# Optimization experiments

Hardware: AMD Instinct MI355X
Metric: run time of the kernel (lower is better)

## Reference

```python
import jax, jax.numpy as jnp
import numpy as np

B, C, N, V, W, D = 4, 64, 8, 32, 32, 256  # spa_dim = D


def _ln(x, g, b, eps=1e-5):
    m = jnp.mean(x, -1, keepdims=True)
    v = jnp.mean((x - m) ** 2, -1, keepdims=True)
    return (x - m) * jax.lax.rsqrt(v + eps) * g + b


def _tokens(x):
    # (b, c, n, v, w) -> (b*n, v*w, c)
    b, c, n, v, w = x.shape
    return x.transpose(0, 2, 3, 4, 1).reshape(b * n, v * w, c)


def setup_inputs() -> dict:
    key = jax.random.key(0)
    ks = jax.random.split(key, 8)
    fea_lf = jax.random.normal(ks[0], (B, C, N, V, W), jnp.float32)
    fea_hf = jax.random.normal(ks[1], (B, C, N, V, W), jnp.float32)
    W_in = jax.random.normal(ks[2], (C, D), jnp.float32) / np.sqrt(C)
    W_kv = jax.random.normal(ks[3], (C, 2 * D), jnp.float32) / np.sqrt(C)
    gamma = jnp.ones((D,), jnp.float32)
    beta = jnp.zeros((D,), jnp.float32)
    g2 = jnp.ones((D,), jnp.float32)
    b2 = jnp.zeros((D,), jnp.float32)
    W1 = jax.random.normal(ks[4], (D, 2 * D), jnp.float32) / np.sqrt(D)
    W2 = jax.random.normal(ks[5], (2 * D, D), jnp.float32) / np.sqrt(2 * D)
    W_out = jax.random.normal(ks[6], (D, C), jnp.float32) / np.sqrt(D)
    return {"fea_lf": fea_lf, "fea_hf": fea_hf, "W_in": W_in, "W_kv": W_kv,
            "gamma": gamma, "beta": beta, "g2": g2, "b2": b2,
            "W1": W1, "W2": W2, "W_out": W_out}


def reference(fea_lf, fea_hf, W_in, W_kv, gamma, beta, g2, b2, W1, W2, W_out):
    b, c, n, v, w = fea_lf.shape
    S = v * w
    tok_q = _tokens(fea_lf)   # (bn, S, c)
    tok_kv = _tokens(fea_hf)  # (bn, S, c)
    q = _ln(tok_q @ W_in, gamma, beta)              # (bn, S, D)
    kv = tok_kv @ W_kv
    k, vtok = jnp.split(kv, 2, axis=-1)
    k = _ln(k, gamma, beta)                          # shared LayerNorm (self.norm)
    # NOTE: original has no 1/sqrt(d) scaling on scores.
    score = jnp.einsum('bqd,bkd->bqk', q, k)         # (bn, S, S)
    mask = jnp.tril(jnp.ones((S, S), bool))
    score = jnp.where(mask, score, jnp.float32(-1e15))
    p = jax.nn.softmax(score, axis=-1)
    att = jnp.einsum('bqk,bkd->bqd', p, vtok)        # (bn, S, D)
    h = jax.nn.relu(_ln(att, g2, b2) @ W1) @ W2      # FFN (dropout=0)
    epi = h + vtok
    out = epi @ W_out                                # (bn, S, c)
    return out.reshape(b, n, v, w, c).transpose(0, 4, 1, 2, 3)
```

## Files before the change

### kernel.cpp

```cpp
#include <hip/hip_runtime.h>

typedef short bf16x8 __attribute__((ext_vector_type(8)));
typedef _Float16 f16x8 __attribute__((ext_vector_type(8)));
typedef float f32x4 __attribute__((ext_vector_type(4)));
typedef unsigned short u16;
typedef unsigned short u16x4 __attribute__((ext_vector_type(4)));

#define MFMA(a, b, c) __builtin_amdgcn_mfma_f32_16x16x32_bf16(a, b, c, 0, 0, 0)
#define MFMAH(a, b, c) __builtin_amdgcn_mfma_f32_16x16x32_f16(a, b, c, 0, 0, 0)

__device__ __forceinline__ u16 f2b(float f) {
    union { float f; unsigned u; } x{f};
    unsigned r = (x.u + 0x7FFFu + ((x.u >> 16) & 1u)) >> 16;
    return (u16)r;
}
__device__ __forceinline__ float b2f(u16 h) {
    union { unsigned u; float f; } x{((unsigned)h) << 16};
    return x.f;
}
__device__ __forceinline__ u16 f2h(float f) {
    _Float16 h = (_Float16)f;
    return *reinterpret_cast<u16*>(&h);
}
__device__ __forceinline__ float h2f(u16 h) {
    _Float16 v = *reinterpret_cast<_Float16*>(&h);
    return (float)v;
}
__device__ __forceinline__ float red16_sum(float v) {
#pragma unroll
    for (int m = 1; m < 16; m <<= 1) v += __shfl_xor(v, m, 64);
    return v;
}
__device__ __forceinline__ float red16_max(float v) {
#pragma unroll
    for (int m = 1; m < 16; m <<= 1) v = fmaxf(v, __shfl_xor(v, m, 64));
    return v;
}
__device__ __forceinline__ void gl_lds16(const void* g, void* l) {
    __builtin_amdgcn_global_load_lds(
        (const __attribute__((address_space(1))) unsigned int*)(g),
        (__attribute__((address_space(3))) unsigned int*)(l), 16, 0, 0);
}


__global__ __launch_bounds__(256) void wconv_kernel(
    const float* __restrict__ W1, const float* __restrict__ W2,
    const float* __restrict__ Wo, const float* __restrict__ Win,
    const float* __restrict__ Wkv, u16* __restrict__ w1T,
    u16* __restrict__ w2T, u16* __restrict__ woT, u16* __restrict__ wfrag) {
    int id = blockIdx.x * 256 + threadIdx.x;
    if (id < 131072) {
        int n = id >> 8, k = id & 255;
        w1T[id] = f2b(W1[k * 512 + n]);
    } else if (id < 262144) {
        int j = id - 131072;
        int n = j >> 9, k = j & 511;
        w2T[j] = f2b(W2[k * 256 + n]);
    } else if (id < 278528) {
        int j = id - 262144;
        int n = j >> 8, k = j & 255;
        woT[j] = f2b(Wo[k * 64 + n]);
    } else if (id < 290816) {
        int fid = id - 278528;
        int arr = fid >> 11;
        int e = fid & 2047;
        int ntck = e >> 6, ln = e & 63;
        int lr = ln & 15, lg2 = ln >> 4;
        int nt = ntck >> 1, ck = ntck & 1;
        int d = nt * 16 + lr;
#pragma unroll
        for (int j = 0; j < 8; j++) {
            int c = ck * 32 + lg2 * 8 + j;
            float x;
            if (arr < 2)       x = Win[c * 256 + d];
            else if (arr < 4)  x = Wkv[c * 512 + d];
            else               x = Wkv[c * 512 + 256 + d];
            u16 h = f2b(x);
            u16 v = (arr & 1) ? f2b(x - b2f(h)) : h;
            wfrag[arr * 16384 + e * 8 + j] = v;
        }
    }
}

#define PJ_AH 0
#define PJ_AL 16384
#define PJ_WREG 32768
#define PJ_WORK 98304
__global__ __launch_bounds__(512, 1) void proj_kernel(
    const float* __restrict__ lf, const float* __restrict__ hf,
    const u16* __restrict__ wqg, const u16* __restrict__ wkg,
    const u16* __restrict__ wvg, const float* __restrict__ gamma,
    const float* __restrict__ beta, u16* __restrict__ qf_,
    u16* __restrict__ kf_, u16* __restrict__ vT) {
    extern __shared__ char sm[];
    const int tid = threadIdx.x;
    const int wave = tid >> 6, lane = tid & 63, lr = lane & 15, lg = lane >> 4;
    const int st = blockIdx.x, bn = blockIdx.y;
    const int b = bn >> 3, n = bn & 7;
    const int s0 = st * 128;
    const size_t baseF = (size_t)b * 524288 + (size_t)n * 1024 + s0;

    float gam[16], bet[16];
#pragma unroll
    for (int nt = 0; nt < 16; nt++) {
        gam[nt] = gamma[nt * 16 + lr];
        bet[nt] = beta[nt * 16 + lr];
    }

    auto stage32 = [&](const float* srcbase, int chalf) {
#pragma unroll
        for (int call = 0; call < 2; call++) {
            int unit = call * 8 + wave;
            int obase = unit << 10;
            int e = unit * 256 + lane * 4;
            int cl = e >> 7, si = e & 127;
            gl_lds16(srcbase + (size_t)(chalf * 32 + cl) * 8192 + si,
                     sm + PJ_WORK + obase);
        }
    };
    auto stageW = [&](const u16* wsrc) {
#pragma unroll
        for (int call = 0; call < 8; call++) {
            int obase = (call * 8 + wave) << 10;
            gl_lds16((const char*)wsrc + obase + lane * 16, sm + PJ_WREG + obase);
        }
    };
    auto buildA = [&](int slotbase) {
        int g = wave >> 1;
        int s = ((wave & 1) << 6) | lane;
        float x[8];
#pragma unroll
        for (int cc = 0; cc < 8; cc++)
            x[cc] = *(const float*)(sm + PJ_WORK + ((g * 8 + cc) << 9) + (s << 2));
        bf16x8 ph, pl;
#pragma unroll
        for (int cc = 0; cc < 8; cc++) {
            u16 h = f2b(x[cc]);
            ph[cc] = (short)h;
            pl[cc] = (short)f2b(x[cc] - b2f(h));
        }
        int slp = (slotbase + g) ^ (s & 7);
        *(bf16x8*)(sm + PJ_AH + (s << 7) + (slp << 4)) = ph;
        *(bf16x8*)(sm + PJ_AL + (s << 7) + (slp << 4)) = pl;
    };
    auto loadA = [&](bf16x8* aH, bf16x8* aL) {
        int tl = wave * 16 + lr;
#pragma unroll
        for (int ck = 0; ck < 2; ck++) {
            int off = (tl << 7) + ((((ck << 2) | lg) ^ (tl & 7)) << 4);
            aH[ck] = *(const bf16x8*)(sm + PJ_AH + off);
            aL[ck] = *(const bf16x8*)(sm + PJ_AL + off);
        }
    };
    auto pass3 = [&](const bf16x8* aH, const bf16x8* aL, f32x4* acc) {
#pragma unroll
        for (int nt = 0; nt < 16; nt++) acc[nt] = (f32x4){0.f, 0.f, 0.f, 0.f};
#pragma unroll
        for (int nt = 0; nt < 16; nt++) {
#pragma unroll
            for (int ck = 0; ck < 2; ck++) {
                int wo = (((nt << 1) | ck) << 10) + (lane << 4);
                bf16x8 bh = *(const bf16x8*)(sm + PJ_WREG + wo);
                bf16x8 bl = *(const bf16x8*)(sm + PJ_WREG + 32768 + wo);
                acc[nt] = MFMA(aH[ck], bh, acc[nt]);
                acc[nt] = MFMA(aL[ck], bh, acc[nt]);
                acc[nt] = MFMA(aH[ck], bl, acc[nt]);
            }
        }
    };
    auto lnstats = [&](const f32x4* acc, float* mean, float* rs) {
#pragma unroll
        for (int r = 0; r < 4; r++) {
            float s1 = 0.f, s2 = 0.f;
#pragma unroll
            for (int nt = 0; nt < 16; nt++) {
                float xv = acc[nt][r];
                s1 += xv; s2 += xv * xv;
            }
            s1 = red16_sum(s1);
            s2 = red16_sum(s2);
            float mn = s1 * (1.f / 256.f);
            float var = s2 * (1.f / 256.f) - mn * mn;
            mean[r] = mn;
            rs[r] = rsqrtf(var + 1e-5f);
        }
    };
    auto emit = [&](const f32x4* acc, const float* mean, const float* rs,
                    u16* dst) {
        char* bw = sm + PJ_WORK + wave * 4096;
        const int gtok = bn * 1024 + s0 + wave * 16;
#pragma unroll
        for (int hh = 0; hh < 2; hh++) {
#pragma unroll
            for (int ntl = 0; ntl < 8; ntl++) {
                int nt = hh * 8 + ntl;
#pragma unroll
                for (int r = 0; r < 4; r++) {
                    float y = (acc[nt][r] - mean[r]) * rs[r] * gam[nt] + bet[nt];
                    int tl = lg * 4 + r;
                    int dl = ntl * 16 + lr;
                    int sl = dl >> 3;
                    *(u16*)(bw + tl * 256 + ((sl ^ ((tl >> 2) & 3)) << 4) +
                            (dl & 7) * 2) = f2h(y);
                }
            }
#pragma unroll
            for (int p = 0; p < 4; p++) {
                int row = lane >> 2, slq = (lane & 3) + p * 4;
                bf16x8 v8 = *(const bf16x8*)(bw + row * 256 +
                                             ((slq ^ ((row >> 2) & 3)) << 4));
                *(bf16x8*)(dst + (size_t)(gtok + row) * 256 + hh * 128 +
                           slq * 8) = v8;
            }
        }
    };

    f32x4 acc[16];
    float mean[4], rs[4];
    bf16x8 aH[2], aL[2];

    stage32(lf + baseF, 0);  __syncthreads();
    buildA(0);               __syncthreads();
    stage32(lf + baseF, 1);
    stageW(wqg);             __syncthreads();
    buildA(4);               __syncthreads();
    loadA(aH, aL);
    pass3(aH, aL, acc);
    lnstats(acc, mean, rs);  __syncthreads();
    stageW(wkg);
    emit(acc, mean, rs, qf_);
    __syncthreads();
    stage32(hf + baseF, 0);  __syncthreads();
    buildA(0);               __syncthreads();
    stage32(hf + baseF, 1);  __syncthreads();
    buildA(4);               __syncthreads();
    loadA(aH, aL);
    pass3(aH, aL, acc);
    lnstats(acc, mean, rs);  __syncthreads();
    stageW(wvg);
    emit(acc, mean, rs, kf_);
    __syncthreads();
    pass3(aH, aL, acc);
#pragma unroll
    for (int nt = 0; nt < 16; nt++) {
        u16x4 pv;
#pragma unroll
        for (int r = 0; r < 4; r++) pv[r] = f2h(acc[nt][r]);
        *(u16x4*)(vT + ((size_t)(bn * 256) + nt * 16 + lr) * 1024 + s0 +
                  wave * 16 + lg * 4) = pv;
    }
}

__global__ __launch_bounds__(256) void attn_kernel(
    const u16* __restrict__ qf_, const u16* __restrict__ kf_,
    const u16* __restrict__ vT, const float* __restrict__ g2,
    const float* __restrict__ b2, u16* __restrict__ lnatt) {
    extern __shared__ char smem[];
    const int tid = threadIdx.x;
    const int wave = tid >> 6, lane = tid & 63, lr = lane & 15, lg = lane >> 4;
    const int idx = blockIdx.x;
    const int j = idx & 255;
    const int bn = j & 31, si = j >> 5;
    const int strip = (idx >= 256) ? (15 - si) : si;
    const int qr0 = strip * 64 + wave * 16;
    const int nk = 2 * strip + 2;
    u16* Pw = (u16*)(smem + 65536 + wave * 1280);

    f16x8 qf[8];
    {
        const size_t off = ((size_t)(bn * 1024 + qr0 + lr)) * 256 + lg * 8;
#pragma unroll
        for (int ck = 0; ck < 8; ck++)
            qf[ck] = *(const f16x8*)(qf_ + off + ck * 32);
    }
    f16x8 onesb;
    {
        _Float16 v1 = (lr == 0) ? (_Float16)1.0f : (_Float16)0.0f;
#pragma unroll
        for (int q = 0; q < 8; q++) onesb[q] = v1;
    }

    const int srl = lane >> 5, ss = lane & 31;
    const int vdl = lane >> 2, vg = lane & 3;
    auto stage = [&](int buf, int kt) {
        const int kv0 = kt << 5;
        char* baseK = smem + buf * 16384;
        char* baseV = smem + 32768 + buf * 16384;
#pragma unroll
        for (int ii = 0; ii < 4; ii++) {
            int u = wave * 4 + ii;
            int r = u * 2 + srl;
            size_t go = (((size_t)((bn << 10) + kv0 + r)) << 8) +
                        (unsigned)((ss ^ (r & 7)) << 3);
            gl_lds16(kf_ + go, baseK + u * 1024);
            int d = u * 16 + vdl;
            size_t gv = (((size_t)((bn << 8) + d)) << 10) + kv0 +
                        (unsigned)((vg ^ ((d >> 1) & 3)) << 3);
            gl_lds16(vT + gv, baseV + u * 1024);
        }
    };

    f32x4 o[16];
#pragma unroll
    for (int i = 0; i < 16; i++) o[i] = (f32x4){0.f, 0.f, 0.f, 0.f};
    f32x4 ol = (f32x4){0.f, 0.f, 0.f, 0.f};
    float m[4] = {-INFINITY, -INFINITY, -INFINITY, -INFINITY};

    stage(0, 0);
    __syncthreads();
    for (int kt = 0; kt < nk; kt++) {
        const int cur = kt & 1;
        if (kt + 1 < nk) stage(cur ^ 1, kt + 1);
        if ((kt << 5) <= qr0 + 15) {
            const char* kb = smem + cur * 16384;
            f32x4 sc0 = (f32x4){0.f, 0.f, 0.f, 0.f};
            f32x4 sc1 = (f32x4){0.f, 0.f, 0.f, 0.f};
#pragma unroll
            for (int ck = 0; ck < 8; ck++) {
                int sw = ((ck * 4 + lg) ^ (lr & 7)) << 4;
                int a0 = lr * 512 + sw;
                f16x8 k0 = *(const f16x8*)(kb + a0);
                f16x8 k1 = *(const f16x8*)(kb + a0 + 8192);
                sc0 = MFMAH(qf[ck], k0, sc0);
                sc1 = MFMAH(qf[ck], k1, sc1);
            }
            float scl[4];
            const int kvb = kt << 5;
#pragma unroll
            for (int r = 0; r < 4; r++) {
                int qi = qr0 + lg * 4 + r;
                float s0v = (kvb + lr > qi) ? -1e30f : sc0[r];
                float s1v = (kvb + 16 + lr > qi) ? -1e30f : sc1[r];
                float tm = red16_max(fmaxf(s0v, s1v));
                float mn = fmaxf(m[r], tm);
                scl[r] = __expf(m[r] - mn);
                m[r] = mn;
                int row = lg * 4 + r;
                Pw[row * 40 + lr] = f2h(__expf(s0v - mn));
                Pw[row * 40 + 16 + lr] = f2h(__expf(s1v - mn));
            }
#pragma unroll
            for (int f = 0; f < 16; f++) {
                f32x4 t = o[f];
                t[0] *= scl[0]; t[1] *= scl[1]; t[2] *= scl[2]; t[3] *= scl[3];
                o[f] = t;
            }
            ol[0] *= scl[0]; ol[1] *= scl[1]; ol[2] *= scl[2]; ol[3] *= scl[3];
            f16x8 pa = *(const f16x8*)((const char*)Pw + lr * 80 + lg * 16);
            const char* vb = smem + 32768 + cur * 16384;
#pragma unroll
            for (int db = 0; db < 16; db++) {
                int d = db * 16 + lr;
                f16x8 vf = *(const f16x8*)(vb + d * 64 +
                                           ((lg ^ ((lr >> 1) & 3)) << 4));
                o[db] = MFMAH(pa, vf, o[db]);
            }
            ol = MFMAH(pa, onesb, ol);
        }
        __syncthreads();
    }
    float linv[4];
#pragma unroll
    for (int r = 0; r < 4; r++) linv[r] = 1.f / __shfl(ol[r], lane & 48, 64);
#pragma unroll
    for (int f = 0; f < 16; f++) {
        o[f][0] *= linv[0]; o[f][1] *= linv[1];
        o[f][2] *= linv[2]; o[f][3] *= linv[3];
    }
    float gv[16], bv[16];
#pragma unroll
    for (int f = 0; f < 16; f++) {
        gv[f] = g2[f * 16 + lr];
        bv[f] = b2[f * 16 + lr];
    }
#pragma unroll
    for (int r = 0; r < 4; r++) {
        float s1 = 0.f, s2 = 0.f;
#pragma unroll
        for (int f = 0; f < 16; f++) { float x = o[f][r]; s1 += x; s2 += x * x; }
        s1 = red16_sum(s1);
        s2 = red16_sum(s2);
        float mean = s1 * (1.f / 256.f);
        float var = s2 * (1.f / 256.f) - mean * mean;
        float rsv = rsqrtf(var + 1e-5f);
        size_t row = (size_t)(bn * 1024 + qr0 + lg * 4 + r) * 256;
#pragma unroll
        for (int f = 0; f < 16; f++)
            lnatt[row + f * 16 + lr] = f2b((o[f][r] - mean) * rsv * gv[f] + bv[f]);
    }
}

template <int K, int NB, int MODE>
__global__ __launch_bounds__(512) void gemmB_kernel(
    const u16* __restrict__ A, const u16* __restrict__ BT,
    u16* __restrict__ outb, const u16* __restrict__ vTr,
    float* __restrict__ outf, int ldOut) {
    extern __shared__ char bsm[];
    const int tid = threadIdx.x;
    const int wave = tid >> 6, lane = tid & 63, lr = lane & 15, lg = lane >> 4;
    constexpr int K2 = K * 2;
    constexpr int BN = NB * 16;
    constexpr int TILE = BN * K2;
    const int m0 = blockIdx.x * 128 + wave * 16;
    const int n0 = blockIdx.y * BN;
    {
        const char* bsrc = (const char*)(BT + (size_t)n0 * K);
        constexpr int ITER = TILE / (512 * 16);
#pragma unroll
        for (int it = 0; it < ITER; it++) {
            int o = (it * 512 + tid) * 16;
            int col = o / K2;
            int slot = (o % K2) >> 4;
            int src = col * K2 + ((slot ^ (col & 7)) << 4);
            gl_lds16(bsrc + src, bsm + o);
        }
    }
    __syncthreads();
    f32x4 acc[NB];
#pragma unroll
    for (int nb = 0; nb < NB; nb++) acc[nb] = (f32x4){0.f, 0.f, 0.f, 0.f};
    const u16* ap = A + (size_t)(m0 + lr) * K + lg * 8;
#pragma unroll
    for (int kc = 0; kc < K; kc += 32) {
        bf16x8 a = *(const bf16x8*)(ap + kc);
        int ks = (kc >> 3) + lg;
#pragma unroll
        for (int nb = 0; nb < NB; nb++) {
            int c = nb * 16 + lr;
            bf16x8 bv = *(const bf16x8*)(bsm + c * K2 + ((ks ^ (c & 7)) << 4));
            acc[nb] = MFMA(a, bv, acc[nb]);
        }
    }
    const int g = m0 + lg * 4;
    if (MODE == 0) {
#pragma unroll
        for (int nb = 0; nb < NB; nb++)
#pragma unroll
            for (int r = 0; r < 4; r++)
                outb[(size_t)(g + r) * ldOut + n0 + nb * 16 + lr] =
                    f2b(fmaxf(acc[nb][r], 0.f));
    } else if (MODE == 1) {
        int bn = g >> 10, s = g & 1023;
#pragma unroll
        for (int nb = 0; nb < NB; nb++) {
            int dd = n0 + nb * 16 + lr;
            u16x4 vv = *(const u16x4*)(vTr + ((size_t)bn * 256 + dd) * 1024 + s);
#pragma unroll
            for (int r = 0; r < 4; r++)
                outb[(size_t)(g + r) * 256 + dd] = f2b(acc[nb][r] + h2f(vv[r]));
        }
    } else {
        int bn = g >> 10, s = g & 1023;
        int bb = bn >> 3, nn = bn & 7;
#pragma unroll
        for (int nb = 0; nb < NB; nb++) {
            int cc = n0 + nb * 16 + lr;
            *(f32x4*)(outf + (size_t)bb * 524288 + (size_t)cc * 8192 +
                      (size_t)nn * 1024 + s) = acc[nb];
        }
    }
}

extern "C" void kernel_launch(void* const* d_in, const int* in_sizes, int n_in,
                              void* d_out, int out_size, void* d_ws, size_t ws_size,
                              hipStream_t stream) {
    const float* lf    = (const float*)d_in[0];
    const float* hf    = (const float*)d_in[1];
    const float* Win   = (const float*)d_in[2];
    const float* Wkv   = (const float*)d_in[3];
    const float* gamma = (const float*)d_in[4];
    const float* beta  = (const float*)d_in[5];
    const float* g2    = (const float*)d_in[6];
    const float* b2    = (const float*)d_in[7];
    const float* W1    = (const float*)d_in[8];
    const float* W2    = (const float*)d_in[9];
    const float* Wo    = (const float*)d_in[10];
    float* out = (float*)d_out;

    char* w = (char*)d_ws;
    const size_t MB16 = 16777216;
    u16* qf  = (u16*)(w);
    u16* kf  = (u16*)(w + MB16);
    u16* vT  = (u16*)(w + 2 * MB16);
    u16* hb  = (u16*)(w + 3 * MB16);
    u16* w1T = (u16*)(w + 3 * MB16 + 33554432);
    u16* w2T = w1T + 131072;
    u16* woT = w2T + 131072;
    u16* wfrag = woT + 16384;
    u16* wqg = wfrag;
    u16* wkg = wfrag + 32768;
    u16* wvg = wfrag + 65536;
    u16* lnatt = qf;
    u16* epib  = kf;

    wconv_kernel<<<dim3(1136), dim3(256), 0, stream>>>(W1, W2, Wo, Win, Wkv,
                                                       w1T, w2T, woT, wfrag);
    proj_kernel<<<dim3(8, 32), dim3(512), 131072, stream>>>(
        lf, hf, wqg, wkg, wvg, gamma, beta, qf, kf, vT);
    attn_kernel<<<dim3(512), dim3(256), 70656, stream>>>(qf, kf, vT, g2, b2,
                                                         lnatt);
    gemmB_kernel<256, 8, 0><<<dim3(256, 4), dim3(512), 65536, stream>>>(
        lnatt, w1T, hb, nullptr, nullptr, 512);
    gemmB_kernel<512, 8, 1><<<dim3(256, 2), dim3(512), 131072, stream>>>(
        hb, w2T, epib, vT, nullptr, 256);
    gemmB_kernel<256, 4, 2><<<dim3(256, 1), dim3(512), 32768, stream>>>(
        epib, woT, nullptr, nullptr, out, 64);
}
```

Baseline: 149.7 us.

## Split causal attention KV range across two wave groups per block and merge

```diff
diff --git a/kernel.cpp b/kernel.cpp
--- a/kernel.cpp
+++ b/kernel.cpp
@@ -251,20 +251,23 @@
     }
 }
 
-__global__ __launch_bounds__(256) void attn_kernel(
+__global__ __launch_bounds__(512) void attn_kernel(
     const u16* __restrict__ qf_, const u16* __restrict__ kf_,
     const u16* __restrict__ vT, const float* __restrict__ g2,
     const float* __restrict__ b2, u16* __restrict__ lnatt) {
     extern __shared__ char smem[];
     const int tid = threadIdx.x;
     const int wave = tid >> 6, lane = tid & 63, lr = lane & 15, lg = lane >> 4;
-    const int idx = blockIdx.x;
-    const int j = idx & 255;
-    const int bn = j & 31, si = j >> 5;
-    const int strip = (idx >= 256) ? (15 - si) : si;
-    const int qr0 = strip * 64 + wave * 16;
-    const int nk = 2 * strip + 2;
-    u16* Pw = (u16*)(smem + 65536 + wave * 1280);
+    const int grp = wave >> 2, w4 = wave & 3;
+    const int b = blockIdx.x;
+    const int bn = b & 31;
+    const int strip = 15 - (b >> 5);
+    const int qr0 = strip * 64 + w4 * 16;
+    const int ni = strip + 1;
+    const int ktbase = grp * ni;
+    char* myK = smem + grp * 65536;
+    char* myV = smem + grp * 65536 + 32768;
+    u16* Pw = (u16*)(smem + 131072 + wave * 1280);
 
     f16x8 qf[8];
     {
@@ -284,11 +287,11 @@
     const int vdl = lane >> 2, vg = lane & 3;
     auto stage = [&](int buf, int kt) {
         const int kv0 = kt << 5;
-        char* baseK = smem + buf * 16384;
-        char* baseV = smem + 32768 + buf * 16384;
+        char* baseK = myK + buf * 16384;
+        char* baseV = myV + buf * 16384;
 #pragma unroll
         for (int ii = 0; ii < 4; ii++) {
-            int u = wave * 4 + ii;
+            int u = w4 * 4 + ii;
             int r = u * 2 + srl;
             size_t go = (((size_t)((bn << 10) + kv0 + r)) << 8) +
                         (unsigned)((ss ^ (r & 7)) << 3);
@@ -306,15 +309,17 @@
     f32x4 ol = (f32x4){0.f, 0.f, 0.f, 0.f};
     float m[4] = {-INFINITY, -INFINITY, -INFINITY, -INFINITY};
 
-    stage(0, 0);
+    stage(0, ktbase);
     __syncthreads();
-    for (int kt = 0; kt < nk; kt++) {
-        const int cur = kt & 1;
-        if (kt + 1 < nk) stage(cur ^ 1, kt + 1);
+    for (int it = 0; it < ni; it++) {
+        const int cur = it & 1;
+        if (it + 1 < ni) stage(cur ^ 1, ktbase + it + 1);
+        const int kt = ktbase + it;
         if ((kt << 5) <= qr0 + 15) {
-            const char* kb = smem + cur * 16384;
+            const char* kb = myK + cur * 16384;
             f32x4 sc0 = (f32x4){0.f, 0.f, 0.f, 0.f};
             f32x4 sc1 = (f32x4){0.f, 0.f, 0.f, 0.f};
+            __builtin_amdgcn_s_setprio(1);
 #pragma unroll
             for (int ck = 0; ck < 8; ck++) {
                 int sw = ((ck * 4 + lg) ^ (lr & 7)) << 4;
@@ -324,6 +329,7 @@
                 sc0 = MFMAH(qf[ck], k0, sc0);
                 sc1 = MFMAH(qf[ck], k1, sc1);
             }
+            __builtin_amdgcn_s_setprio(0);
             float scl[4];
             const int kvb = kt << 5;
 #pragma unroll
@@ -347,7 +353,8 @@
             }
             ol[0] *= scl[0]; ol[1] *= scl[1]; ol[2] *= scl[2]; ol[3] *= scl[3];
             f16x8 pa = *(const f16x8*)((const char*)Pw + lr * 80 + lg * 16);
-            const char* vb = smem + 32768 + cur * 16384;
+            const char* vb = myV + cur * 16384;
+            __builtin_amdgcn_s_setprio(1);
 #pragma unroll
             for (int db = 0; db < 16; db++) {
                 int d = db * 16 + lr;
@@ -356,37 +363,76 @@
                 o[db] = MFMAH(pa, vf, o[db]);
             }
             ol = MFMAH(pa, onesb, ol);
+            __builtin_amdgcn_s_setprio(0);
         }
         __syncthreads();
     }
-    float linv[4];
-#pragma unroll
-    for (int r = 0; r < 4; r++) linv[r] = 1.f / __shfl(ol[r], lane & 48, 64);
-#pragma unroll
-    for (int f = 0; f < 16; f++) {
-        o[f][0] *= linv[0]; o[f][1] *= linv[1];
-        o[f][2] *= linv[2]; o[f][3] *= linv[3];
-    }
-    float gv[16], bv[16];
-#pragma unroll
-    for (int f = 0; f < 16; f++) {
-        gv[f] = g2[f * 16 + lr];
-        bv[f] = b2[f * 16 + lr];
-    }
-#pragma unroll
-    for (int r = 0; r < 4; r++) {
-        float s1 = 0.f, s2 = 0.f;
-#pragma unroll
-        for (int f = 0; f < 16; f++) { float x = o[f][r]; s1 += x; s2 += x * x; }
-        s1 = red16_sum(s1);
-        s2 = red16_sum(s2);
-        float mean = s1 * (1.f / 256.f);
-        float var = s2 * (1.f / 256.f) - mean * mean;
-        float rsv = rsqrtf(var + 1e-5f);
-        size_t row = (size_t)(bn * 1024 + qr0 + lg * 4 + r) * 256;
+    float lsum[4];
+#pragma unroll
+    for (int r = 0; r < 4; r++) lsum[r] = __shfl(ol[r], lane & 48, 64);
+
+    char* cb = smem + 65536;
+    float* mlb = (float*)(smem + 131072);
+    if (grp == 1) {
+        char* po = cb + w4 * 16384;
 #pragma unroll
         for (int f = 0; f < 16; f++)
-            lnatt[row + f * 16 + lr] = f2b((o[f][r] - mean) * rsv * gv[f] + bv[f]);
+            *(f32x4*)(po + (f * 16 + lr) * 64 + lg * 16) = o[f];
+        if (lr == 0) {
+#pragma unroll
+            for (int r = 0; r < 4; r++) {
+                int row = lg * 4 + r;
+                mlb[(w4 * 16 + row) * 2] = m[r];
+                mlb[(w4 * 16 + row) * 2 + 1] = lsum[r];
+            }
+        }
+    }
+    __syncthreads();
+    if (grp == 0) {
+        const char* po = cb + w4 * 16384;
+        float e0[4], e1[4], linv[4];
+#pragma unroll
+        for (int r = 0; r < 4; r++) {
+            int row = lg * 4 + r;
+            float m1 = mlb[(w4 * 16 + row) * 2];
+            float l1 = mlb[(w4 * 16 + row) * 2 + 1];
+            float ms = fmaxf(m[r], m1);
+            e0[r] = __expf(m[r] - ms);
+            e1[r] = __expf(m1 - ms);
+            linv[r] = 1.f / (lsum[r] * e0[r] + l1 * e1[r]);
+        }
+#pragma unroll
+        for (int f = 0; f < 16; f++) {
+            f32x4 o1 = *(const f32x4*)(po + (f * 16 + lr) * 64 + lg * 16);
+#pragma unroll
+            for (int r = 0; r < 4; r++)
+                o[f][r] = (o[f][r] * e0[r] + o1[r] * e1[r]) * linv[r];
+        }
+        float gv[16], bv[16];
+#pragma unroll
+        for (int f = 0; f < 16; f++) {
+            gv[f] = g2[f * 16 + lr];
+            bv[f] = b2[f * 16 + lr];
+        }
+#pragma unroll
+        for (int r = 0; r < 4; r++) {
+            float s1 = 0.f, s2 = 0.f;
+#pragma unroll
+            for (int f = 0; f < 16; f++) {
+                float x = o[f][r];
+                s1 += x; s2 += x * x;
+            }
+            s1 = red16_sum(s1);
+            s2 = red16_sum(s2);
+            float mean = s1 * (1.f / 256.f);
+            float var = s2 * (1.f / 256.f) - mean * mean;
+            float rsv = rsqrtf(var + 1e-5f);
+            size_t row = (size_t)(bn * 1024 + qr0 + lg * 4 + r) * 256;
+#pragma unroll
+            for (int f = 0; f < 16; f++)
+                lnatt[row + f * 16 + lr] =
+                    f2b((o[f][r] - mean) * rsv * gv[f] + bv[f]);
+        }
     }
 }
 
@@ -497,8 +543,8 @@
                                                        w1T, w2T, woT, wfrag);
     proj_kernel<<<dim3(8, 32), dim3(512), 131072, stream>>>(
         lf, hf, wqg, wkg, wvg, gamma, beta, qf, kf, vT);
-    attn_kernel<<<dim3(512), dim3(256), 70656, stream>>>(qf, kf, vT, g2, b2,
-                                                         lnatt);
+    attn_kernel<<<dim3(512), dim3(512), 141312, stream>>>(qf, kf, vT, g2, b2,
+                                                          lnatt);
     gemmB_kernel<256, 8, 0><<<dim3(256, 4), dim3(512), 65536, stream>>>(
         lnatt, w1T, hb, nullptr, nullptr, 512);
     gemmB_kernel<512, 8, 1><<<dim3(256, 2), dim3(512), 131072, stream>>>(
```

Result: faster. 135.1 us (-9.8%).
